# Performance work log

Hardware: AMD Instinct MI355X
Metric: run time of the kernel (lower is better)

## Reference

```python
import jax, jax.numpy as jnp
import numpy as np
from jax import lax

B, T, N, NIN, NOUT = 16, 32, 512, 32, 16
STEEP_GJ, STEEP_FIRE, STEEP_IN = 10.0, 10.0, 5.0
INPUT_THRESH, LEAKY_SLOPE = 0.01, 0.01
EDGE_P = 0.05


def setup_inputs() -> dict:
    key = jax.random.key(0)
    ks = jax.random.split(key, 7)
    obs_sequence = jax.random.normal(ks[0], (B, T, NIN), dtype=jnp.float32)
    weights = jax.random.uniform(ks[1], (N, N), dtype=jnp.float32) * 5.0
    thresholds = jax.random.uniform(ks[2], (N,), dtype=jnp.float32) * 5.0
    decay = jax.random.uniform(ks[3], (N,), dtype=jnp.float32) * 0.5
    mask_ex = jax.random.bernoulli(ks[4], EDGE_P, (N, N)).astype(jnp.float32)
    mask_in = jax.random.bernoulli(ks[5], EDGE_P, (N, N)).astype(jnp.float32)
    mask_gj = jax.random.bernoulli(ks[6], EDGE_P, (N, N)).astype(jnp.float32)
    input_indices = jnp.arange(NIN, dtype=jnp.int32)
    output_indices = NIN + jnp.arange(NOUT, dtype=jnp.int32)
    return {"obs_sequence": obs_sequence, "weights": weights, "thresholds": thresholds,
            "decay": decay, "mask_ex": mask_ex, "mask_in": mask_in, "mask_gj": mask_gj,
            "input_indices": input_indices, "output_indices": output_indices}


def reference(obs_sequence, weights, thresholds, decay, mask_ex, mask_in, mask_gj,
              input_indices, output_indices):
    # obs_encoder and action_decoder are identity: obs values drive input neurons,
    # action = E-state of output neurons.
    W_pos = jax.nn.softplus(weights)            # [N,N] (dst, src)
    W_chem = W_pos * (mask_ex - mask_in)        # excitatory minus inhibitory
    W_gj = W_pos * mask_gj                      # gap junctions

    def step(carry, obs_t):
        E, O = carry                            # [B,N] each
        O_h = O.at[:, input_indices].set(obs_t)
        E_h = E.at[:, input_indices].set(obs_t)
        # chemical synapse current: [B,N] @ [N,N]^T
        I_chem = O_h @ W_chem.T
        # gap junction current via O(B,N,N) broadcast, as in original
        diff = O_h[:, None, :] - E_h[:, :, None]          # [B, dst, src]
        direction = jnp.tanh(STEEP_GJ * diff)
        I_gj = jnp.einsum('ds,bs,bds->bd', W_gj, O_h, direction)
        curr = jnp.clip(E_h + I_chem + I_gj, -10.0, 10.0)
        z = curr - thresholds
        O_new = jnp.where(z >= 0, z, LEAKY_SLOPE * z)      # leaky_relu
        firing_gate = jax.nn.sigmoid(STEEP_FIRE * z)
        decay_gate = jax.nn.sigmoid(STEEP_IN * (jnp.abs(E_h - curr) - INPUT_THRESH))
        E_nonfired = decay_gate * curr + (1.0 - decay_gate) * (E_h - decay)
        E_new = firing_gate * O_new + (1.0 - firing_gate) * E_nonfired
        O_new = O_new.at[:, input_indices].set(obs_t)
        E_new = E_new.at[:, input_indices].set(obs_t)
        action = E_new[:, output_indices]
        return (E_new, O_new), action

    b, n = obs_sequence.shape[0], weights.shape[0]
    E0 = jnp.zeros((b, n), dtype=obs_sequence.dtype)
    O0 = jnp.zeros((b, n), dtype=obs_sequence.dtype)
    (_, _), actions = lax.scan(step, (E0, O0), jnp.swapaxes(obs_sequence, 0, 1))
    return jnp.swapaxes(actions, 0, 1)                    # [B,T,NOUT]
```

## Files before the change

kernel.cpp:

```cpp
#include <hip/hip_runtime.h>

#define N_NEUR 512
#define B_SZ   16
#define T_STEPS 32
#define NIN    32
#define NOUT   16
#define CAPC   84
#define CAPG   52
#define MC     42
#define MG     26
#define MCP    21
#define MGP    13
#define LOG2E  1.4426950408889634f

__device__ __forceinline__ float rcp_fast(float x) {
#if __has_builtin(__builtin_amdgcn_rcpf)
    return __builtin_amdgcn_rcpf(x);
#else
    return 1.0f / x;
#endif
}
__device__ __forceinline__ float exp2_fast(float x) {
#if __has_builtin(__builtin_amdgcn_exp2f)
    return __builtin_amdgcn_exp2f(x);
#else
    return exp2f(x);
#endif
}

__global__ __launch_bounds__(64) void prep1_kernel(
    const float* __restrict__ W,
    const float* __restrict__ mex,
    const float* __restrict__ min_,
    const float* __restrict__ mgj,
    int* __restrict__ key_arr, int* __restrict__ ccA, int* __restrict__ cgA,
    int2* __restrict__ tmpC, int2* __restrict__ tmpG)
{
    const int row  = blockIdx.x;
    const int lane = threadIdx.x;
    const unsigned long long below = (1ull << lane) - 1ull;
    int bc = 0, bg = 0;
    for (int c0 = 0; c0 < N_NEUR; c0 += 64) {
        const int col = c0 + lane;
        const int off = row * N_NEUR + col;
        const float w  = W[off];
        const float sp = fmaxf(w, 0.0f) + log1pf(__expf(-fabsf(w)));
        const float dm = mex[off] - min_[off];
        bool a = (dm != 0.0f);
        unsigned long long m = __ballot(a);
        int idx = bc + __popcll(m & below);
        if (a && idx < CAPC)
            tmpC[row * CAPC + idx] = make_int2(col, __float_as_int(sp * dm));
        bc += __popcll(m);

        const float g = mgj[off];
        bool ag = (g != 0.0f);
        m = __ballot(ag);
        idx = bg + __popcll(m & below);
        if (ag && idx < CAPG)
            tmpG[row * CAPG + idx] = make_int2(col, __float_as_int(sp * g));
        bg += __popcll(m);
    }
    if (lane == 0) {
        int cc = min(bc, CAPC), cg = min(bg, CAPG);
        ccA[row] = cc; cgA[row] = cg; key_arr[row] = cc + cg;
    }
}

__global__ __launch_bounds__(64) void prep2_kernel(
    const int* __restrict__ key_arr, const int* __restrict__ ccA, const int* __restrict__ cgA,
    const int2* __restrict__ tmpC, const int2* __restrict__ tmpG,
    int* __restrict__ order,
    float* __restrict__ wCt, unsigned* __restrict__ cpCt,
    float* __restrict__ wGt, unsigned* __restrict__ cpGt)
{
    __shared__ int colC[CAPC];
    __shared__ int colG[CAPG];
    const int d    = blockIdx.x;
    const int lane = threadIdx.x;
    const int kd   = key_arr[d];
    int r = 0;
    for (int j = lane; j < N_NEUR; j += 64) {
        int kj = key_arr[j];
        r += (kj < kd) || (kj == kd && j < d);
    }
    #pragma unroll
    for (int i = 1; i < 64; i <<= 1) r += __shfl_xor(r, i);
    if (lane == 0) order[r] = d;

    const int wv = r >> 5;
    const int Lb = 2 * (r & 31);
    const int cc = ccA[d], cg = cgA[d];

    for (int k = lane; k < CAPC; k += 64) colC[k] = 0;
    for (int k = lane; k < CAPG; k += 64) colG[k] = 0;
    __syncthreads();
    for (int k = lane; k < cc; k += 64) colC[k] = tmpC[d * CAPC + k].x;
    for (int k = lane; k < cg; k += 64) colG[k] = tmpG[d * CAPG + k].x;

    for (int s = lane; s < CAPC; s += 64) {
        float w = (s < cc) ? __int_as_float(tmpC[d * CAPC + s].y) : 0.0f;
        wCt[(wv * MC + (s >> 1)) * 64 + Lb + (s & 1)] = w;
    }
    for (int s = lane; s < CAPG; s += 64) {
        float w = (s < cg) ? __int_as_float(tmpG[d * CAPG + s].y) : 0.0f;
        wGt[(wv * MG + (s >> 1)) * 64 + Lb + (s & 1)] = w;
    }
    __syncthreads();
    for (int u = lane; u < 2 * MCP; u += 64) {
        int kp = u >> 1, h = u & 1;
        unsigned c0 = (unsigned)colC[4 * kp + h] << 2;
        unsigned c1 = (unsigned)colC[4 * kp + 2 + h] << 2;
        cpCt[(wv * MCP + kp) * 64 + Lb + h] = c0 | (c1 << 16);
    }
    for (int u = lane; u < 2 * MGP; u += 64) {
        int kp = u >> 1, h = u & 1;
        unsigned c0 = (unsigned)colG[4 * kp + h] << 2;
        unsigned c1 = (unsigned)colG[4 * kp + 2 + h] << 2;
        cpGt[(wv * MGP + kp) * 64 + Lb + h] = c0 | (c1 << 16);
    }
}

#define CHEM_K(k) {                                                         \
    unsigned pk = cpC[(k) >> 1];                                            \
    unsigned off = ((k) & 1) ? (pk >> 16) : (pk & 0xffffu);                 \
    acc = fmaf(wC[k], *(const float*)((const char*)ObP + off), acc); }

#define GJ_K(k) {                                                           \
    unsigned pk = cpG[(k) >> 1];                                            \
    unsigned off = ((k) & 1) ? (pk >> 16) : (pk & 0xffffu);                 \
    float Os = *(const float*)((const char*)ObP + off);                     \
    float f = fmaf(20.0f * LOG2E, Os, cE);                                  \
    float tnh = 1.0f - 2.0f * rcp_fast(1.0f + exp2_fast(f));                \
    acc = fmaf(wG[k] * Os, tnh, acc); }

__global__ __launch_bounds__(1024, 1) void recur_kernel(
    const float* __restrict__ obs,
    const float* __restrict__ thr,
    const float* __restrict__ dec,
    const int* __restrict__ order, const int* __restrict__ ccA, const int* __restrict__ cgA,
    const float* __restrict__ wCt, const unsigned* __restrict__ cpCt,
    const float* __restrict__ wGt, const unsigned* __restrict__ cpGt,
    float* __restrict__ out)
{
    __shared__ float Ob[2][N_NEUR];
    __shared__ float Eb[2][N_NEUR];

    const int b    = blockIdx.x;
    const int tid  = threadIdx.x;
    const int h    = tid & 1;
    const int r    = tid >> 1;
    const int wv   = tid >> 6;
    const int lane = tid & 63;

    const int d = order[r];
    const int cc = ccA[d];
    const int cg = cgA[d];
    const float thr_d = thr[d];
    const float dec_d = dec[d];

    int ccw = cc, cgw = cg;
    #pragma unroll
    for (int i = 1; i < 64; i <<= 1) {
        ccw = max(ccw, __shfl_xor(ccw, i));
        cgw = max(cgw, __shfl_xor(cgw, i));
    }
    const int mCw = __builtin_amdgcn_readfirstlane((ccw + 1) >> 1);
    const int mGw = __builtin_amdgcn_readfirstlane((cgw + 1) >> 1);

    float wC[MC]; unsigned cpC[MCP];
    float wG[MG]; unsigned cpG[MGP];
    #pragma unroll
    for (int k = 0; k < MC; ++k)  wC[k]  = wCt[(wv * MC + k) * 64 + lane];
    #pragma unroll
    for (int k = 0; k < MCP; ++k) cpC[k] = cpCt[(wv * MCP + k) * 64 + lane];
    #pragma unroll
    for (int k = 0; k < MG; ++k)  wG[k]  = wGt[(wv * MG + k) * 64 + lane];
    #pragma unroll
    for (int k = 0; k < MGP; ++k) cpG[k] = cpGt[(wv * MGP + k) * 64 + lane];

    if (h == 0) { Ob[0][d] = 0.0f; Eb[0][d] = 0.0f; }
    const bool wr = (h == 0) && (d >= NIN) && (d < NIN + NOUT);
    float* outp = out + (size_t)b * T_STEPS * NOUT + (d - NIN);
    const float* obs_b = obs + b * (T_STEPS * NIN);
    const bool inj = (h == 0) && (d < NIN);
    float ob_next = inj ? obs_b[d] : 0.0f;
    int p = 0;
    __syncthreads();

    for (int t = 0; t < T_STEPS; ++t) {
        if (inj) {
            Ob[p][d] = ob_next;
            Eb[p][d] = ob_next;
        }
        __syncthreads();
        float ob_pf = (t + 1 < T_STEPS && inj) ? obs_b[(t + 1) * NIN + d] : 0.0f;

        const float* ObP = Ob[p];
        const float E_d = Eb[p][d];
        float acc = 0.0f;
        { CHEM_K(0) CHEM_K(1) CHEM_K(2) CHEM_K(3) CHEM_K(4) CHEM_K(5) CHEM_K(6) CHEM_K(7) }
        if (8 < mCw)  { CHEM_K(8)  CHEM_K(9)  CHEM_K(10) CHEM_K(11) CHEM_K(12) CHEM_K(13) CHEM_K(14) CHEM_K(15) }
        if (16 < mCw) { CHEM_K(16) CHEM_K(17) CHEM_K(18) CHEM_K(19) CHEM_K(20) CHEM_K(21) CHEM_K(22) CHEM_K(23) }
        if (24 < mCw) { CHEM_K(24) CHEM_K(25) CHEM_K(26) CHEM_K(27) CHEM_K(28) CHEM_K(29) CHEM_K(30) CHEM_K(31) }
        if (32 < mCw) { CHEM_K(32) CHEM_K(33) CHEM_K(34) CHEM_K(35) CHEM_K(36) CHEM_K(37) CHEM_K(38) CHEM_K(39) }
        if (40 < mCw) { CHEM_K(40) CHEM_K(41) }
        const float cE = -20.0f * LOG2E * E_d;
        { GJ_K(0) GJ_K(1) GJ_K(2) GJ_K(3) GJ_K(4) GJ_K(5) GJ_K(6) GJ_K(7) }
        if (8 < mGw)  { GJ_K(8)  GJ_K(9)  GJ_K(10) GJ_K(11) GJ_K(12) GJ_K(13) GJ_K(14) GJ_K(15) }
        if (16 < mGw) { GJ_K(16) GJ_K(17) GJ_K(18) GJ_K(19) GJ_K(20) GJ_K(21) GJ_K(22) GJ_K(23) }
        if (24 < mGw) { GJ_K(24) GJ_K(25) }

        acc += __shfl_xor(acc, 1);

        float curr = fminf(fmaxf(E_d + acc, -10.0f), 10.0f);
        float z = curr - thr_d;
        float O_new = (z >= 0.0f) ? z : 0.01f * z;
        float fg = rcp_fast(1.0f + exp2_fast(-10.0f * LOG2E * z));
        float dg = rcp_fast(1.0f + exp2_fast(-5.0f * LOG2E * (fabsf(E_d - curr) - 0.01f)));
        float E_nf  = dg * curr + (1.0f - dg) * (E_d - dec_d);
        float E_new = fg * O_new + (1.0f - fg) * E_nf;

        const int q = p ^ 1;
        if (h == 0) {
            Eb[q][d] = E_new;
            Ob[q][d] = O_new;
            if (wr) outp[t * NOUT] = E_new;
        }
        ob_next = ob_pf;
        __syncthreads();
        p = q;
    }
}

extern "C" void kernel_launch(void* const* d_in, const int* in_sizes, int n_in,
                              void* d_out, int out_size, void* d_ws, size_t ws_size,
                              hipStream_t stream)
{
    const float* obs  = (const float*)d_in[0];
    const float* W    = (const float*)d_in[1];
    const float* thr  = (const float*)d_in[2];
    const float* dec  = (const float*)d_in[3];
    const float* mex  = (const float*)d_in[4];
    const float* min_ = (const float*)d_in[5];
    const float* mgj  = (const float*)d_in[6];
    float* out = (float*)d_out;

    char* ws = (char*)d_ws;
    int*   key_arr = (int*)(ws);
    int*   ccA     = (int*)(ws + 2048);
    int*   cgA     = (int*)(ws + 4096);
    int*   order   = (int*)(ws + 6144);
    int2*  tmpC    = (int2*)(ws + 8192);
    int2*  tmpG    = (int2*)(ws + 8192 + 344064);
    float* wCt     = (float*)(ws + 565248);
    unsigned* cpCt = (unsigned*)(ws + 737280);
    float* wGt     = (float*)(ws + 823296);
    unsigned* cpGt = (unsigned*)(ws + 929792);

    prep1_kernel<<<N_NEUR, 64, 0, stream>>>(W, mex, min_, mgj,
                                            key_arr, ccA, cgA, tmpC, tmpG);
    prep2_kernel<<<N_NEUR, 64, 0, stream>>>(key_arr, ccA, cgA, tmpC, tmpG,
                                            order, wCt, cpCt, wGt, cpGt);
    recur_kernel<<<B_SZ, 1024, 0, stream>>>(obs, thr, dec,
                                            order, ccA, cgA,
                                            wCt, cpCt, wGt, cpGt, out);
}
```

Baseline: 185.4 us.

## Sort synapse columns to avoid LDS bank conflicts, drop per-step barrier, split accumulators

The prep kernel now sorts each row's synapse entries by a bank-rotated key relative to the lane's position, so the gathers from the shared O buffer in the recurrent loop hit distinct LDS banks more often. The recurrent loop folds observation injection into the end-of-step write, which removes one __syncthreads per timestep. It also uses two alternating accumulators for finer-grained early exit and more ILP. The sort is serial in four lanes per block, which adds prep cost, and the different summation order can change floating-point rounding slightly.

```diff
diff --git a/kernel.cpp b/kernel.cpp
--- a/kernel.cpp
+++ b/kernel.cpp
@@ -74,8 +74,8 @@
     float* __restrict__ wCt, unsigned* __restrict__ cpCt,
     float* __restrict__ wGt, unsigned* __restrict__ cpGt)
 {
-    __shared__ int colC[CAPC];
-    __shared__ int colG[CAPG];
+    __shared__ int   cS[CAPC];  __shared__ float wS[CAPC];
+    __shared__ int   cSg[CAPG]; __shared__ float wSg[CAPG];
     const int d    = blockIdx.x;
     const int lane = threadIdx.x;
     const int kd   = key_arr[d];
@@ -92,47 +92,66 @@
     const int Lb = 2 * (r & 31);
     const int cc = ccA[d], cg = cgA[d];
 
-    for (int k = lane; k < CAPC; k += 64) colC[k] = 0;
-    for (int k = lane; k < CAPG; k += 64) colG[k] = 0;
+    for (int k = lane; k < CAPC; k += 64) {
+        int2 e = (k < cc) ? tmpC[d * CAPC + k] : make_int2(0, 0);
+        cS[k] = e.x; wS[k] = __int_as_float(e.y);
+    }
+    for (int k = lane; k < CAPG; k += 64) {
+        int2 e = (k < cg) ? tmpG[d * CAPG + k] : make_int2(0, 0);
+        cSg[k] = e.x; wSg[k] = __int_as_float(e.y);
+    }
     __syncthreads();
-    for (int k = lane; k < cc; k += 64) colC[k] = tmpC[d * CAPC + k].x;
-    for (int k = lane; k < cg; k += 64) colG[k] = tmpG[d * CAPG + k].x;
-
-    for (int s = lane; s < CAPC; s += 64) {
-        float w = (s < cc) ? __int_as_float(tmpC[d * CAPC + s].y) : 0.0f;
-        wCt[(wv * MC + (s >> 1)) * 64 + Lb + (s & 1)] = w;
-    }
-    for (int s = lane; s < CAPG; s += 64) {
-        float w = (s < cg) ? __int_as_float(tmpG[d * CAPG + s].y) : 0.0f;
-        wGt[(wv * MG + (s >> 1)) * 64 + Lb + (s & 1)] = w;
-    }
-    __syncthreads();
-    for (int u = lane; u < 2 * MCP; u += 64) {
-        int kp = u >> 1, h = u & 1;
-        unsigned c0 = (unsigned)colC[4 * kp + h] << 2;
-        unsigned c1 = (unsigned)colC[4 * kp + 2 + h] << 2;
-        cpCt[(wv * MCP + kp) * 64 + Lb + h] = c0 | (c1 << 16);
-    }
-    for (int u = lane; u < 2 * MGP; u += 64) {
-        int kp = u >> 1, h = u & 1;
-        unsigned c0 = (unsigned)colG[4 * kp + h] << 2;
-        unsigned c1 = (unsigned)colG[4 * kp + 2 + h] << 2;
-        cpGt[(wv * MGP + kp) * 64 + Lb + h] = c0 | (c1 << 16);
-    }
-}
-
-#define CHEM_K(k) {                                                         \
+
+    if (lane < 4) {
+        const int isG = lane >> 1, h = lane & 1;
+        const int cnt = isG ? cg : cc;
+        const int M   = isG ? MG : MC;
+        const int MP  = isG ? MGP : MCP;
+        const int myL = Lb + h;
+        int cols[MC]; float ws[MC];
+        int m = 0;
+        for (int s = h; s < cnt; s += 2) {
+            cols[m] = isG ? cSg[s] : cS[s];
+            ws[m]   = isG ? wSg[s] : wS[s];
+            ++m;
+        }
+        for (int i = 1; i < m; ++i) {
+            int c = cols[i]; float w = ws[i];
+            int key = ((c & 31) - myL) & 31;
+            int j = i - 1;
+            while (j >= 0 && ((((cols[j] & 31) - myL) & 31) > key)) {
+                cols[j + 1] = cols[j]; ws[j + 1] = ws[j]; --j;
+            }
+            cols[j + 1] = c; ws[j + 1] = w;
+        }
+        float*    wT = isG ? wGt  : wCt;
+        unsigned* cT = isG ? cpGt : cpCt;
+        for (int k = 0; k < M; ++k)
+            wT[(wv * M + k) * 64 + myL] = (k < m) ? ws[k] : 0.0f;
+        for (int kp = 0; kp < MP; ++kp) {
+            unsigned c0 = (2 * kp     < m) ? ((unsigned)cols[2 * kp]     << 2) : 0u;
+            unsigned c1 = (2 * kp + 1 < m) ? ((unsigned)cols[2 * kp + 1] << 2) : 0u;
+            cT[(wv * MP + kp) * 64 + myL] = c0 | (c1 << 16);
+        }
+    }
+}
+
+#define CHEM_K(k, A) {                                                      \
     unsigned pk = cpC[(k) >> 1];                                            \
     unsigned off = ((k) & 1) ? (pk >> 16) : (pk & 0xffffu);                 \
-    acc = fmaf(wC[k], *(const float*)((const char*)ObP + off), acc); }
-
-#define GJ_K(k) {                                                           \
+    A = fmaf(wC[k], *(const float*)((const char*)ObP + off), A); }
+
+#define CHEM_C4(a) { CHEM_K(a, accA) CHEM_K((a)+1, accB) CHEM_K((a)+2, accA) CHEM_K((a)+3, accB) }
+
+#define GJ_K(k, A) {                                                        \
     unsigned pk = cpG[(k) >> 1];                                            \
     unsigned off = ((k) & 1) ? (pk >> 16) : (pk & 0xffffu);                 \
     float Os = *(const float*)((const char*)ObP + off);                     \
     float f = fmaf(20.0f * LOG2E, Os, cE);                                  \
     float tnh = 1.0f - 2.0f * rcp_fast(1.0f + exp2_fast(f));                \
-    acc = fmaf(wG[k] * Os, tnh, acc); }
+    A = fmaf(wG[k] * Os, tnh, A); }
+
+#define GJ_C4(a) { GJ_K(a, accA) GJ_K((a)+1, accB) GJ_K((a)+2, accA) GJ_K((a)+3, accB) }
 
 __global__ __launch_bounds__(1024, 1) void recur_kernel(
     const float* __restrict__ obs,
@@ -179,38 +198,46 @@
     #pragma unroll
     for (int k = 0; k < MGP; ++k) cpG[k] = cpGt[(wv * MGP + k) * 64 + lane];
 
-    if (h == 0) { Ob[0][d] = 0.0f; Eb[0][d] = 0.0f; }
-    const bool wr = (h == 0) && (d >= NIN) && (d < NIN + NOUT);
+    const bool inj = (h == 0) && (d < NIN);
+    const bool wr  = (h == 0) && (d >= NIN) && (d < NIN + NOUT);
     float* outp = out + (size_t)b * T_STEPS * NOUT + (d - NIN);
     const float* obs_b = obs + b * (T_STEPS * NIN);
-    const bool inj = (h == 0) && (d < NIN);
-    float ob_next = inj ? obs_b[d] : 0.0f;
+
+    if (h == 0) {
+        float v = (d < NIN) ? obs_b[d] : 0.0f;
+        Ob[0][d] = v;
+        Eb[0][d] = v;
+    }
     int p = 0;
     __syncthreads();
 
     for (int t = 0; t < T_STEPS; ++t) {
-        if (inj) {
-            Ob[p][d] = ob_next;
-            Eb[p][d] = ob_next;
-        }
-        __syncthreads();
-        float ob_pf = (t + 1 < T_STEPS && inj) ? obs_b[(t + 1) * NIN + d] : 0.0f;
+        float ob_next = (inj && (t + 1 < T_STEPS)) ? obs_b[(t + 1) * NIN + d] : 0.0f;
 
         const float* ObP = Ob[p];
         const float E_d = Eb[p][d];
-        float acc = 0.0f;
-        { CHEM_K(0) CHEM_K(1) CHEM_K(2) CHEM_K(3) CHEM_K(4) CHEM_K(5) CHEM_K(6) CHEM_K(7) }
-        if (8 < mCw)  { CHEM_K(8)  CHEM_K(9)  CHEM_K(10) CHEM_K(11) CHEM_K(12) CHEM_K(13) CHEM_K(14) CHEM_K(15) }
-        if (16 < mCw) { CHEM_K(16) CHEM_K(17) CHEM_K(18) CHEM_K(19) CHEM_K(20) CHEM_K(21) CHEM_K(22) CHEM_K(23) }
-        if (24 < mCw) { CHEM_K(24) CHEM_K(25) CHEM_K(26) CHEM_K(27) CHEM_K(28) CHEM_K(29) CHEM_K(30) CHEM_K(31) }
-        if (32 < mCw) { CHEM_K(32) CHEM_K(33) CHEM_K(34) CHEM_K(35) CHEM_K(36) CHEM_K(37) CHEM_K(38) CHEM_K(39) }
-        if (40 < mCw) { CHEM_K(40) CHEM_K(41) }
+        float accA = 0.0f, accB = 0.0f;
+        CHEM_C4(0)
+        if ( 4 < mCw) CHEM_C4(4)
+        if ( 8 < mCw) CHEM_C4(8)
+        if (12 < mCw) CHEM_C4(12)
+        if (16 < mCw) CHEM_C4(16)
+        if (20 < mCw) CHEM_C4(20)
+        if (24 < mCw) CHEM_C4(24)
+        if (28 < mCw) CHEM_C4(28)
+        if (32 < mCw) CHEM_C4(32)
+        if (36 < mCw) CHEM_C4(36)
+        if (40 < mCw) { CHEM_K(40, accA) CHEM_K(41, accB) }
         const float cE = -20.0f * LOG2E * E_d;
-        { GJ_K(0) GJ_K(1) GJ_K(2) GJ_K(3) GJ_K(4) GJ_K(5) GJ_K(6) GJ_K(7) }
-        if (8 < mGw)  { GJ_K(8)  GJ_K(9)  GJ_K(10) GJ_K(11) GJ_K(12) GJ_K(13) GJ_K(14) GJ_K(15) }
-        if (16 < mGw) { GJ_K(16) GJ_K(17) GJ_K(18) GJ_K(19) GJ_K(20) GJ_K(21) GJ_K(22) GJ_K(23) }
-        if (24 < mGw) { GJ_K(24) GJ_K(25) }
-
+        GJ_C4(0)
+        if ( 4 < mGw) GJ_C4(4)
+        if ( 8 < mGw) GJ_C4(8)
+        if (12 < mGw) GJ_C4(12)
+        if (16 < mGw) GJ_C4(16)
+        if (20 < mGw) GJ_C4(20)
+        if (24 < mGw) { GJ_K(24, accA) GJ_K(25, accB) }
+
+        float acc = accA + accB;
         acc += __shfl_xor(acc, 1);
 
         float curr = fminf(fmaxf(E_d + acc, -10.0f), 10.0f);
@@ -223,11 +250,10 @@
 
         const int q = p ^ 1;
         if (h == 0) {
-            Eb[q][d] = E_new;
-            Ob[q][d] = O_new;
+            Eb[q][d] = inj ? ob_next : E_new;
+            Ob[q][d] = inj ? ob_next : O_new;
             if (wr) outp[t * NOUT] = E_new;
         }
-        ob_next = ob_pf;
         __syncthreads();
         p = q;
     }
```

Result: slower. 295.7 us (+59.5%).
